# Performance work log

Measured on AMD Instinct MI355X. Metric: run time of the kernel, lower is better.

## Reference

```python
import jax, jax.numpy as jnp
import numpy as np
import math

B, S, HQ, HK, D, GH, BLK = 2, 8192, 32, 8, 128, 128, 64
NB = S // BLK          # 128 key blocks
G = HQ // HK           # gqa group size = 4


def _rope_tables(n, dim):
    inv_freq = 1.0 / (10000.0 ** (np.arange(0, dim, 2, dtype=np.float64) / dim))
    t = np.arange(n, dtype=np.float64)
    freqs = np.outer(t, inv_freq)              # [n, dim/2]
    emb = np.concatenate([freqs, freqs], axis=-1)  # [n, dim]
    return (jnp.asarray(np.cos(emb), jnp.float32),
            jnp.asarray(np.sin(emb), jnp.float32))


def rotate_half(x):
    h = x.shape[-1] // 2
    return jnp.concatenate([-x[..., h:], x[..., :h]], axis=-1)


def setup_inputs() -> dict:
    key = jax.random.key(0)
    kq, kk, kwq, kwk = jax.random.split(key, 4)
    q = jax.random.normal(kq, (B, S, HQ, D), jnp.float32)
    k = jax.random.normal(kk, (B, S, HK, D), jnp.float32)
    # xavier-uniform-ish init for the gate weights
    lim_q = math.sqrt(6.0 / (G * D + GH))
    wq = jax.random.uniform(kwq, (HK, G, D, GH), jnp.float32, -lim_q, lim_q)
    lim_k = math.sqrt(6.0 / (2 * D + GH))
    wk = jax.random.uniform(kwk, (HK, 2 * D, GH), jnp.float32, -lim_k, lim_k)
    # additive float causal block mask: query s may attend to block j iff j <= s // BLK
    pos = jnp.arange(S)[:, None] // BLK        # [S,1]
    blk = jnp.arange(NB)[None, :]              # [1,NB]
    mask = jnp.where(blk <= pos, 0.0, -1e9).astype(jnp.float32)  # [S,NB]
    attention_mask = jnp.broadcast_to(mask[None, None], (B, 1, S, NB))
    cos_s, sin_s = _rope_tables(S, GH)         # [S,GH]
    cos_b, sin_b = _rope_tables(NB, GH)        # [NB,GH]
    cos_q = jnp.broadcast_to(cos_s[None], (B, S, GH))
    sin_q = jnp.broadcast_to(sin_s[None], (B, S, GH))
    cos_k = jnp.broadcast_to(cos_b[None], (B, NB, GH))
    sin_k = jnp.broadcast_to(sin_b[None], (B, NB, GH))
    return {"q": q, "k": k, "attention_mask": attention_mask,
            "cos_q": cos_q, "sin_q": sin_q, "cos_k": cos_k, "sin_k": sin_k,
            "wq": wq, "wk": wk}


def reference(q, k, attention_mask, cos_q, sin_q, cos_k, sin_k, wq, wk):
    kh, g, d, gh = wq.shape
    b, s, hq, _ = q.shape
    nb = cos_k.shape[1]
    blk = s // nb
    # --- Q path: head-grouped projection (Qproj) ---
    qg = q.reshape(b, s, kh, g, d)
    qp = jnp.einsum('bskgi,kgio->bsko', qg, wq)        # [b,s,kh,gh]
    qp = qp.transpose(0, 2, 1, 3)                      # [b,kh,s,gh]
    qp = qp * cos_q[:, None] + rotate_half(qp) * sin_q[:, None]
    # --- K path: block pooling (avg + max), multi-head projection ---
    kb = k.reshape(b, nb, blk, kh, d)                  # blocks of BLK keys
    kc = jnp.concatenate([kb.mean(axis=2), kb.max(axis=2)], axis=-1)  # [b,nb,kh,2d]
    kp = jnp.einsum('bnhi,hio->bnho', kc, wk)          # [b,nb,kh,gh]
    kp = kp.transpose(0, 2, 1, 3)                      # [b,kh,nb,gh]
    kp = kp * cos_k[:, None] + rotate_half(kp) * sin_k[:, None]
    # --- masked block attention scores ---
    scale = jnp.float32(1.0 / math.sqrt(gh))
    attn = jnp.einsum('bhsg,bhng->bhsn', qp, kp) * scale  # [b,kh,s,nb]
    attn = attn + attention_mask                       # float additive mask branch
    return jax.nn.softmax(attn, axis=-1)
```

## Files before the change

### kernel.cpp

```cpp
#include <hip/hip_runtime.h>
#include <hip/hip_bf16.h>
#include <cstdint>

#define B_   2
#define S_   8192
#define HQ_  32
#define HK_  8
#define D_   128
#define GH_  128
#define NB_  128
#define G_   4
#define KQ_  512

typedef _Float16 half4_t __attribute__((ext_vector_type(4)));
typedef float    f32x4   __attribute__((ext_vector_type(4)));

__global__ void prep_wq(const float* __restrict__ wq, _Float16* __restrict__ wqt) {
    int idx = blockIdx.x * 256 + threadIdx.x;
    int kh = idx >> 16;
    int o  = (idx >> 9) & 127;
    int i  = idx & 511;
    float v = wq[(size_t)(kh * 512 + i) * 128 + o];
    wqt[idx] = (_Float16)v;
}

__global__ void kpath(const float* __restrict__ k, const float* __restrict__ wk,
                      const float* __restrict__ cosk, const float* __restrict__ sink,
                      float* __restrict__ kp_rope) {
    int bid = blockIdx.x;
    int b  = bid >> 10;
    int kh = (bid >> 7) & 7;
    int n  = bid & 127;
    int d  = threadIdx.x;
    __shared__ float kc[256];
    __shared__ float kpv[128];

    const float* kb = k + ((size_t)(b * S_ + n * 64) * HK_ + kh) * D_ + d;
    float sum = 0.f, mx = -INFINITY;
    #pragma unroll 8
    for (int r = 0; r < 64; ++r) {
        float v = kb[(size_t)r * (HK_ * D_)];
        sum += v; mx = fmaxf(mx, v);
    }
    kc[d]       = sum * (1.0f / 64.0f);
    kc[128 + d] = mx;
    __syncthreads();

    const float* wkb = wk + (size_t)(kh * 256) * 128 + d;
    float acc = 0.f;
    #pragma unroll 8
    for (int i = 0; i < 256; ++i) acc += kc[i] * wkb[(size_t)i * 128];
    kpv[d] = acc;
    __syncthreads();

    float rot = (d < 64) ? -kpv[d + 64] : kpv[d - 64];
    float c = cosk[(b * NB_ + n) * 128 + d];
    float s = sink[(b * NB_ + n) * 128 + d];
    kp_rope[((size_t)((b * 8 + kh) * 128 + n)) * 128 + d] = acc * c + rot * s;
}

__global__ __launch_bounds__(512) void fused(
        const float* __restrict__ q, const _Float16* __restrict__ wqt,
        const float* __restrict__ cosq, const float* __restrict__ sinq,
        const float* __restrict__ kp, float* __restrict__ out) {
    int bid = blockIdx.x;
    int b  = bid >> 9;
    int kh = (bid >> 6) & 7;
    int ms = bid & 63;
    int s0 = ms * 128;
    int tid = threadIdx.x;
    int l = tid & 63, w = tid >> 6, q4 = l >> 4;

    __shared__ __align__(16) char buf[65536];
    char*     kpl  = buf;
    char*     qpl  = buf + 32768;
    _Float16* Alds = (_Float16*)(buf + 32768);
    char*     Bb   = buf + 36864;

    int ntmax16 = (((((ms << 1) | 1)) >> 4) + 1) << 4;
    const float* kpg = kp + (size_t)((b * 8 + kh) * 128) * 128;
    #pragma unroll
    for (int m = 0; m < 8; ++m) {
        int flat4 = m * 512 + tid;
        int row = flat4 >> 5;
        if (row < ntmax16) {
            int c4 = (flat4 & 31) * 4;
            f32x4 v = *(const f32x4*)(kpg + row * 128 + c4);
            half4_t h = {(_Float16)v.x, (_Float16)v.y, (_Float16)v.z, (_Float16)v.w};
            *(half4_t*)(kpl + ((row * 256 + c4 * 2) ^ ((row & 7) << 4))) = h;
        }
    }

    f32x4 acc[8];
    #pragma unroll
    for (int t = 0; t < 8; ++t)
        for (int e = 0; e < 4; ++e) acc[t][e] = 0.f;

    int ar = tid >> 2, akk = (tid & 3) * 4;
    const float* qrow = q + (size_t)(b * S_ + s0 + ar) * (HQ_ * D_) + kh * KQ_;
    int bo = tid >> 2, bh = tid & 3;
    const half4_t* wrow = (const half4_t*)(wqt + (size_t)(kh * 128 + bo) * KQ_);

    f32x4   av = *(const f32x4*)(qrow + akk);
    half4_t bv = wrow[bh];

    for (int ks = 0; ks < 32; ++ks) {
        half4_t ah = {(_Float16)av.x, (_Float16)av.y, (_Float16)av.z, (_Float16)av.w};
        *(half4_t*)(Alds + ar * 16 + akk) = ah;
        *(half4_t*)(Bb + ((bo * 32 + bh * 8) ^ ((bo & 7) << 3))) = bv;
        __syncthreads();
        if (ks < 31) {
            av = *(const f32x4*)(qrow + (ks + 1) * 16 + akk);
            bv = wrow[(ks + 1) * 4 + bh];
        }
        int arow = w * 16 + (l & 15);
        half4_t af = *(const half4_t*)(Alds + arow * 16 + q4 * 4);
        #pragma unroll
        for (int t = 0; t < 8; ++t) {
            int brow = t * 16 + (l & 15);
            half4_t bf = *(const half4_t*)(Bb + ((brow * 32 + q4 * 8) ^ ((brow & 7) << 3)));
            acc[t] = __builtin_amdgcn_mfma_f32_16x16x16f16(af, bf, acc[t], 0, 0, 0);
        }
        __syncthreads();
    }

    #pragma unroll
    for (int reg = 0; reg < 4; ++reg) {
        int srow = w * 16 + q4 * 4 + reg;
        const float* crow = cosq + (size_t)(b * S_ + s0 + srow) * GH_;
        const float* srw  = sinq + (size_t)(b * S_ + s0 + srow) * GH_;
        #pragma unroll
        for (int t = 0; t < 8; ++t) {
            int col = t * 16 + (l & 15);
            float rot = (t < 4) ? -acc[t + 4][reg] : acc[t - 4][reg];
            float v = acc[t][reg] * crow[col] + rot * srw[col];
            *(_Float16*)(qpl + ((srow * 256 + col * 2) ^ ((srow & 7) << 4))) = (_Float16)v;
        }
    }
    __syncthreads();

    int thresh = (ms << 1) | (w >> 2);
    int nt = (thresh >> 4) + 1;
    int arow = w * 16 + (l & 15);
    half4_t af[8];
    #pragma unroll
    for (int ks = 0; ks < 8; ++ks)
        af[ks] = *(const half4_t*)(qpl + ((arow * 256 + ks * 32 + q4 * 8) ^ ((arow & 7) << 4)));
    #pragma unroll
    for (int t = 0; t < 8; ++t)
        for (int e = 0; e < 4; ++e) acc[t][e] = 0.f;
    #pragma unroll
    for (int t = 0; t < 8; ++t) {
        if (t < nt) {
            int brow = t * 16 + (l & 15);
            #pragma unroll
            for (int ks = 0; ks < 8; ++ks) {
                half4_t bf = *(const half4_t*)(kpl + ((brow * 256 + ks * 32 + q4 * 8) ^ ((brow & 7) << 4)));
                acc[t] = __builtin_amdgcn_mfma_f32_16x16x16f16(af[ks], bf, acc[t], 0, 0, 0);
            }
        }
    }

    const float scale = 0.08838834764831845f;
    #pragma unroll
    for (int reg = 0; reg < 4; ++reg) {
        int srow = w * 16 + q4 * 4 + reg;
        float v[8];
        float mx = -1e30f;
        #pragma unroll
        for (int t = 0; t < 8; ++t) {
            if (t < nt) {
                int col = t * 16 + (l & 15);
                float x = acc[t][reg] * scale + ((col <= thresh) ? 0.f : -1e9f);
                v[t] = x; mx = fmaxf(mx, x);
            }
        }
        #pragma unroll
        for (int off = 1; off < 16; off <<= 1) mx = fmaxf(mx, __shfl_xor(mx, off));
        float sum = 0.f;
        #pragma unroll
        for (int t = 0; t < 8; ++t) {
            if (t < nt) { v[t] = __expf(v[t] - mx); sum += v[t]; }
        }
        #pragma unroll
        for (int off = 1; off < 16; off <<= 1) sum += __shfl_xor(sum, off);
        float r = 1.0f / sum;
        float* orow = out + (size_t)((b * 8 + kh) * S_ + s0 + srow) * NB_;
        #pragma unroll
        for (int t = 0; t < 8; ++t)
            orow[t * 16 + (l & 15)] = (t < nt) ? v[t] * r : 0.f;
    }
}

extern "C" void kernel_launch(void* const* d_in, const int* in_sizes, int n_in,
                              void* d_out, int out_size, void* d_ws, size_t ws_size,
                              hipStream_t stream) {
    const float* q    = (const float*)d_in[0];
    const float* k    = (const float*)d_in[1];
    const float* cosq = (const float*)d_in[3];
    const float* sinq = (const float*)d_in[4];
    const float* cosk = (const float*)d_in[5];
    const float* sink = (const float*)d_in[6];
    const float* wq   = (const float*)d_in[7];
    const float* wk   = (const float*)d_in[8];
    float* out = (float*)d_out;

    char* ws = (char*)d_ws;
    _Float16* wqt     = (_Float16*)ws;
    float*    kp_rope = (float*)(ws + (1 << 20));

    prep_wq<<<2048, 256, 0, stream>>>(wq, wqt);
    kpath  <<<2048, 128, 0, stream>>>(k, wk, cosk, sink, kp_rope);
    fused  <<<1024, 512, 0, stream>>>(q, wqt, cosq, sinq, kp_rope, out);
}
```

Before: 479.3 us.

## Widen Q-projection K-steps with 16x16x32 MFMA, vectorize prep and kpath kernels

The Q projection GEMM now stages 64-wide K slices per iteration using half8 loads and the 16x16x32 f16 MFMA, which cuts the number of barrier-separated iterations from 32 to 8. The score GEMM also switches to the wider MFMA. The wq transpose kernel becomes an LDS-tiled transpose with vectorized loads and stores. The K pooling kernel uses 256 threads with float4 loads and a two-stage reduction, and splits the projection across two halves. This targets barrier and latency overhead and uncoalesced access, at the cost of more LDS staging space and extra reductions.

```diff
diff --git a/kernel.cpp b/kernel.cpp
--- a/kernel.cpp
+++ b/kernel.cpp
@@ -13,50 +13,95 @@
 #define KQ_  512
 
 typedef _Float16 half4_t __attribute__((ext_vector_type(4)));
+typedef _Float16 half8_t __attribute__((ext_vector_type(8)));
 typedef float    f32x4   __attribute__((ext_vector_type(4)));
 
-__global__ void prep_wq(const float* __restrict__ wq, _Float16* __restrict__ wqt) {
-    int idx = blockIdx.x * 256 + threadIdx.x;
-    int kh = idx >> 16;
-    int o  = (idx >> 9) & 127;
-    int i  = idx & 511;
-    float v = wq[(size_t)(kh * 512 + i) * 128 + o];
-    wqt[idx] = (_Float16)v;
-}
-
-__global__ void kpath(const float* __restrict__ k, const float* __restrict__ wk,
-                      const float* __restrict__ cosk, const float* __restrict__ sink,
-                      float* __restrict__ kp_rope) {
+__global__ __launch_bounds__(256) void prep_wq(const float* __restrict__ wq,
+                                               _Float16* __restrict__ wqt) {
+    int bid = blockIdx.x;
+    int kh = bid >> 2, ic = bid & 3;
+    int tid = threadIdx.x;
+    __shared__ _Float16 tile[128][136];
+
+    int c4 = (tid & 31) * 4, r8 = tid >> 5;
+    const float* src = wq + (size_t)(kh * 512 + ic * 128) * 128;
+    #pragma unroll
+    for (int j = 0; j < 16; ++j) {
+        int i = j * 8 + r8;
+        f32x4 v = *(const f32x4*)(src + (size_t)i * 128 + c4);
+        #pragma unroll
+        for (int e = 0; e < 4; ++e) tile[c4 + e][i] = (_Float16)v[e];
+    }
+    __syncthreads();
+    int o = tid >> 1, ih = (tid & 1) * 64;
+    _Float16* dst = wqt + (size_t)(kh * 128 + o) * 512 + ic * 128 + ih;
+    #pragma unroll
+    for (int m = 0; m < 8; ++m)
+        *(half8_t*)(dst + m * 8) = *(const half8_t*)(&tile[o][ih + m * 8]);
+}
+
+__global__ __launch_bounds__(256) void kpath(
+        const float* __restrict__ k, const float* __restrict__ wk,
+        const float* __restrict__ cosk, const float* __restrict__ sink,
+        float* __restrict__ kp_rope) {
     int bid = blockIdx.x;
     int b  = bid >> 10;
     int kh = (bid >> 7) & 7;
     int n  = bid & 127;
-    int d  = threadIdx.x;
+    int tid = threadIdx.x;
+
+    __shared__ f32x4 ps[8][32];
+    __shared__ f32x4 pm[8][32];
     __shared__ float kc[256];
+    __shared__ float pv[2][128];
     __shared__ float kpv[128];
 
-    const float* kb = k + ((size_t)(b * S_ + n * 64) * HK_ + kh) * D_ + d;
-    float sum = 0.f, mx = -INFINITY;
-    #pragma unroll 8
-    for (int r = 0; r < 64; ++r) {
-        float v = kb[(size_t)r * (HK_ * D_)];
-        sum += v; mx = fmaxf(mx, v);
-    }
-    kc[d]       = sum * (1.0f / 64.0f);
-    kc[128 + d] = mx;
-    __syncthreads();
-
-    const float* wkb = wk + (size_t)(kh * 256) * 128 + d;
+    int c32 = tid & 31, rg = tid >> 5;
+    const float* base = k + ((size_t)(b * S_ + n * 64 + rg) * HK_ + kh) * D_ + c32 * 4;
+    f32x4 s4 = {0.f, 0.f, 0.f, 0.f};
+    f32x4 m4 = {-1e30f, -1e30f, -1e30f, -1e30f};
+    #pragma unroll
+    for (int j = 0; j < 8; ++j) {
+        f32x4 v = *(const f32x4*)(base + (size_t)j * 8 * (HK_ * D_));
+        s4 += v;
+        #pragma unroll
+        for (int e = 0; e < 4; ++e) m4[e] = fmaxf(m4[e], v[e]);
+    }
+    ps[rg][c32] = s4; pm[rg][c32] = m4;
+    __syncthreads();
+    if (tid < 32) {
+        f32x4 s = ps[0][tid], m = pm[0][tid];
+        #pragma unroll
+        for (int r = 1; r < 8; ++r) {
+            s += ps[r][tid];
+            #pragma unroll
+            for (int e = 0; e < 4; ++e) m[e] = fmaxf(m[e], pm[r][tid][e]);
+        }
+        #pragma unroll
+        for (int e = 0; e < 4; ++e) {
+            kc[tid * 4 + e]       = s[e] * (1.0f / 64.0f);
+            kc[128 + tid * 4 + e] = m[e];
+        }
+    }
+    __syncthreads();
+
+    int o = tid & 127, hf = tid >> 7;
+    const float* wkb = wk + ((size_t)(kh * 256 + hf * 128)) * 128 + o;
     float acc = 0.f;
     #pragma unroll 8
-    for (int i = 0; i < 256; ++i) acc += kc[i] * wkb[(size_t)i * 128];
-    kpv[d] = acc;
-    __syncthreads();
-
-    float rot = (d < 64) ? -kpv[d + 64] : kpv[d - 64];
-    float c = cosk[(b * NB_ + n) * 128 + d];
-    float s = sink[(b * NB_ + n) * 128 + d];
-    kp_rope[((size_t)((b * 8 + kh) * 128 + n)) * 128 + d] = acc * c + rot * s;
+    for (int i = 0; i < 128; ++i) acc += kc[hf * 128 + i] * wkb[(size_t)i * 128];
+    pv[hf][o] = acc;
+    __syncthreads();
+    if (tid < 128) kpv[tid] = pv[0][tid] + pv[1][tid];
+    __syncthreads();
+    if (tid < 128) {
+        int d = tid;
+        float v = kpv[d];
+        float rot = (d < 64) ? -kpv[d + 64] : kpv[d - 64];
+        float c = cosk[(b * NB_ + n) * 128 + d];
+        float s = sink[(b * NB_ + n) * 128 + d];
+        kp_rope[((size_t)((b * 8 + kh) * 128 + n)) * 128 + d] = v * c + rot * s;
+    }
 }
 
 __global__ __launch_bounds__(512) void fused(
@@ -69,15 +114,15 @@
     int ms = bid & 63;
     int s0 = ms * 128;
     int tid = threadIdx.x;
-    int l = tid & 63, w = tid >> 6, q4 = l >> 4;
+    int l = tid & 63, w = tid >> 6, hi = l >> 4, lo = l & 15;
 
     __shared__ __align__(16) char buf[65536];
-    char*     kpl  = buf;
-    char*     qpl  = buf + 32768;
-    _Float16* Alds = (_Float16*)(buf + 32768);
-    char*     Bb   = buf + 36864;
-
-    int ntmax16 = (((((ms << 1) | 1)) >> 4) + 1) << 4;
+    char* kpl = buf;
+    char* Ab  = buf + 32768;
+    char* Bb  = buf + 49152;
+    char* qpl = buf + 32768;
+
+    int ntmax16 = ((((ms << 1) | 1) >> 4) + 1) << 4;
     const float* kpg = kp + (size_t)((b * 8 + kh) * 128) * 128;
     #pragma unroll
     for (int m = 0; m < 8; ++m) {
@@ -96,42 +141,60 @@
     for (int t = 0; t < 8; ++t)
         for (int e = 0; e < 4; ++e) acc[t][e] = 0.f;
 
-    int ar = tid >> 2, akk = (tid & 3) * 4;
-    const float* qrow = q + (size_t)(b * S_ + s0 + ar) * (HQ_ * D_) + kh * KQ_;
-    int bo = tid >> 2, bh = tid & 3;
-    const half4_t* wrow = (const half4_t*)(wqt + (size_t)(kh * 128 + bo) * KQ_);
-
-    f32x4   av = *(const f32x4*)(qrow + akk);
-    half4_t bv = wrow[bh];
-
-    for (int ks = 0; ks < 32; ++ks) {
-        half4_t ah = {(_Float16)av.x, (_Float16)av.y, (_Float16)av.z, (_Float16)av.w};
-        *(half4_t*)(Alds + ar * 16 + akk) = ah;
-        *(half4_t*)(Bb + ((bo * 32 + bh * 8) ^ ((bo & 7) << 3))) = bv;
+    int srw_ = tid >> 2;
+    int sc   = (tid & 3) * 16;
+    const float*    qbase = q + (size_t)(b * S_ + s0 + srw_) * (HQ_ * D_) + kh * KQ_ + sc;
+    const _Float16* wbase = wqt + (size_t)(kh * 128 + srw_) * KQ_ + sc;
+    int aoff0 = (srw_ * 128 + sc * 2) ^ ((srw_ & 7) << 4);
+    int aoff1 = (srw_ * 128 + sc * 2 + 16) ^ ((srw_ & 7) << 4);
+
+    f32x4 av[4]; half8_t bv0, bv1;
+    #pragma unroll
+    for (int j = 0; j < 4; ++j) av[j] = *(const f32x4*)(qbase + j * 4);
+    bv0 = *(const half8_t*)(wbase);
+    bv1 = *(const half8_t*)(wbase + 8);
+
+    for (int ks = 0; ks < 8; ++ks) {
+        half8_t ah0, ah1;
+        #pragma unroll
+        for (int e = 0; e < 4; ++e) {
+            ah0[e] = (_Float16)av[0][e]; ah0[4 + e] = (_Float16)av[1][e];
+            ah1[e] = (_Float16)av[2][e]; ah1[4 + e] = (_Float16)av[3][e];
+        }
+        *(half8_t*)(Ab + aoff0) = ah0;
+        *(half8_t*)(Ab + aoff1) = ah1;
+        *(half8_t*)(Bb + aoff0) = bv0;
+        *(half8_t*)(Bb + aoff1) = bv1;
+        if (ks < 7) {
+            #pragma unroll
+            for (int j = 0; j < 4; ++j)
+                av[j] = *(const f32x4*)(qbase + (ks + 1) * 64 + j * 4);
+            bv0 = *(const half8_t*)(wbase + (ks + 1) * 64);
+            bv1 = *(const half8_t*)(wbase + (ks + 1) * 64 + 8);
+        }
         __syncthreads();
-        if (ks < 31) {
-            av = *(const f32x4*)(qrow + (ks + 1) * 16 + akk);
-            bv = wrow[(ks + 1) * 4 + bh];
-        }
-        int arow = w * 16 + (l & 15);
-        half4_t af = *(const half4_t*)(Alds + arow * 16 + q4 * 4);
-        #pragma unroll
-        for (int t = 0; t < 8; ++t) {
-            int brow = t * 16 + (l & 15);
-            half4_t bf = *(const half4_t*)(Bb + ((brow * 32 + q4 * 8) ^ ((brow & 7) << 3)));
-            acc[t] = __builtin_amdgcn_mfma_f32_16x16x16f16(af, bf, acc[t], 0, 0, 0);
+        int arow = w * 16 + lo;
+        #pragma unroll
+        for (int sl = 0; sl < 2; ++sl) {
+            half8_t af = *(const half8_t*)(Ab + ((arow * 128 + sl * 64 + hi * 16) ^ ((arow & 7) << 4)));
+            #pragma unroll
+            for (int t = 0; t < 8; ++t) {
+                int br = t * 16 + lo;
+                half8_t bf = *(const half8_t*)(Bb + ((br * 128 + sl * 64 + hi * 16) ^ ((br & 7) << 4)));
+                acc[t] = __builtin_amdgcn_mfma_f32_16x16x32_f16(af, bf, acc[t], 0, 0, 0);
+            }
         }
         __syncthreads();
     }
 
     #pragma unroll
     for (int reg = 0; reg < 4; ++reg) {
-        int srow = w * 16 + q4 * 4 + reg;
+        int srow = w * 16 + hi * 4 + reg;
         const float* crow = cosq + (size_t)(b * S_ + s0 + srow) * GH_;
         const float* srw  = sinq + (size_t)(b * S_ + s0 + srow) * GH_;
         #pragma unroll
         for (int t = 0; t < 8; ++t) {
-            int col = t * 16 + (l & 15);
+            int col = t * 16 + lo;
             float rot = (t < 4) ? -acc[t + 4][reg] : acc[t - 4][reg];
             float v = acc[t][reg] * crow[col] + rot * srw[col];
             *(_Float16*)(qpl + ((srow * 256 + col * 2) ^ ((srow & 7) << 4))) = (_Float16)v;
@@ -141,22 +204,22 @@
 
     int thresh = (ms << 1) | (w >> 2);
     int nt = (thresh >> 4) + 1;
-    int arow = w * 16 + (l & 15);
-    half4_t af[8];
-    #pragma unroll
-    for (int ks = 0; ks < 8; ++ks)
-        af[ks] = *(const half4_t*)(qpl + ((arow * 256 + ks * 32 + q4 * 8) ^ ((arow & 7) << 4)));
+    int arow = w * 16 + lo;
+    half8_t qf[4];
+    #pragma unroll
+    for (int sl = 0; sl < 4; ++sl)
+        qf[sl] = *(const half8_t*)(qpl + ((arow * 256 + sl * 64 + hi * 16) ^ ((arow & 7) << 4)));
     #pragma unroll
     for (int t = 0; t < 8; ++t)
         for (int e = 0; e < 4; ++e) acc[t][e] = 0.f;
     #pragma unroll
     for (int t = 0; t < 8; ++t) {
         if (t < nt) {
-            int brow = t * 16 + (l & 15);
-            #pragma unroll
-            for (int ks = 0; ks < 8; ++ks) {
-                half4_t bf = *(const half4_t*)(kpl + ((brow * 256 + ks * 32 + q4 * 8) ^ ((brow & 7) << 4)));
-                acc[t] = __builtin_amdgcn_mfma_f32_16x16x16f16(af[ks], bf, acc[t], 0, 0, 0);
+            int br = t * 16 + lo;
+            #pragma unroll
+            for (int sl = 0; sl < 4; ++sl) {
+                half8_t bf = *(const half8_t*)(kpl + ((br * 256 + sl * 64 + hi * 16) ^ ((br & 7) << 4)));
+                acc[t] = __builtin_amdgcn_mfma_f32_16x16x32_f16(qf[sl], bf, acc[t], 0, 0, 0);
             }
         }
     }
@@ -164,13 +227,13 @@
     const float scale = 0.08838834764831845f;
     #pragma unroll
     for (int reg = 0; reg < 4; ++reg) {
-        int srow = w * 16 + q4 * 4 + reg;
+        int srow = w * 16 + hi * 4 + reg;
         float v[8];
         float mx = -1e30f;
         #pragma unroll
         for (int t = 0; t < 8; ++t) {
             if (t < nt) {
-                int col = t * 16 + (l & 15);
+                int col = t * 16 + lo;
                 float x = acc[t][reg] * scale + ((col <= thresh) ? 0.f : -1e9f);
                 v[t] = x; mx = fmaxf(mx, x);
             }
@@ -188,7 +251,7 @@
         float* orow = out + (size_t)((b * 8 + kh) * S_ + s0 + srow) * NB_;
         #pragma unroll
         for (int t = 0; t < 8; ++t)
-            orow[t * 16 + (l & 15)] = (t < nt) ? v[t] * r : 0.f;
+            orow[t * 16 + lo] = (t < nt) ? v[t] * r : 0.f;
     }
 }
 
@@ -209,7 +272,7 @@
     _Float16* wqt     = (_Float16*)ws;
     float*    kp_rope = (float*)(ws + (1 << 20));
 
-    prep_wq<<<2048, 256, 0, stream>>>(wq, wqt);
-    kpath  <<<2048, 128, 0, stream>>>(k, wk, cosk, sink, kp_rope);
+    prep_wq<<<32,   256, 0, stream>>>(wq, wqt);
+    kpath  <<<2048, 256, 0, stream>>>(k, wk, cosk, sink, kp_rope);
     fused  <<<1024, 512, 0, stream>>>(q, wqt, cosq, sinq, kp_rope, out);
 }
```

New measurement: 467.6 us. -2.5%, faster.
